# Kernel optimization log

Measured on AMD Instinct MI355X. Metric: run time of the kernel, lower is better.

## Reference

```python
import jax, jax.numpy as jnp
import numpy as np
from jax.scipy.special import digamma, gammaln

NUM_CLASSES = 3
FOCAL_GAMMA = 2.0
LABEL_SMOOTHING = 0.1
EVIDENTIAL_W = 0.1
CONTRASTIVE_W = 0.1
BOUNDARY_W = 0.15
TRIPLET_W = 0.1
QUALITY_W = 0.1
TRIPLET_MARGIN = 1.5


def setup_inputs() -> dict:
    key = jax.random.key(0)
    k1, k2, k3 = jax.random.split(key, 3)
    B, D = 4096, 512
    logits = jax.random.normal(k1, (B, NUM_CLASSES), dtype=jnp.float32)
    targets = jax.random.randint(k2, (B,), 0, 3)
    features = jax.random.normal(k3, (B, D), dtype=jnp.float32)
    alpha = jax.random.uniform(jax.random.fold_in(key, 7), (B, NUM_CLASSES), dtype=jnp.float32)
    focal_alpha = jnp.array([1.0, 2.0, 1.5], dtype=jnp.float32)
    class_weights = jnp.array([1.0, 2.0, 1.5], dtype=jnp.float32)
    return {"logits": logits, "targets": targets, "features": features,
            "alpha": alpha, "epoch": 1, "focal_alpha": focal_alpha,
            "class_weights": class_weights}


def reference(logits, targets, features, alpha, epoch, focal_alpha, class_weights):
    B = logits.shape[0]
    C = NUM_CLASSES

    # ---- focal loss (label-smoothed CE, torch semantics) ----
    logp = jax.nn.log_softmax(logits, axis=1)                      # [B,C]
    nll = -jnp.take_along_axis(logp, targets[:, None], axis=1)[:, 0]
    ce_ls = (1.0 - LABEL_SMOOTHING) * nll + LABEL_SMOOTHING * (-logp.mean(axis=1))
    pt = jnp.exp(-ce_ls)
    focal = (focal_alpha[targets] * (1.0 - pt) ** FOCAL_GAMMA * ce_ls).mean()

    # ---- weighted CE (torch weighted mean: sum(w*nll)/sum(w)) ----
    w = class_weights[targets]
    ce = (w * nll).sum() / w.sum()

    # ---- enhanced boundary loss ----
    probs = jax.nn.softmax(logits, axis=1)
    real = targets == 0
    semi = targets == 1
    syn = targets == 2
    rb = jnp.where(real, probs[:, 1] + 0.6 * probs[:, 2], 0.0).sum()
    sb = jnp.where(syn, probs[:, 1] + 0.4 * probs[:, 0], 0.0).sum()
    mb = jnp.where(semi, 1.0 - probs[:, 1] + 0.3 * (probs[:, 0] + probs[:, 2]), 0.0).sum()
    boundary = (rb + sb + 4.5 * mb) / (B + 1e-8)

    total = 0.4 * focal + 0.3 * ce + BOUNDARY_W * boundary

    # ---- normalized features and pairwise cosine-sim matrix ----
    norms = jnp.linalg.norm(features, axis=1, keepdims=True)
    f = features / jnp.maximum(norms, 1e-12)
    sim = f @ f.T                                                  # [B,B]
    same = targets[:, None] == targets[None, :]
    eye = jnp.eye(B, dtype=bool)

    # ---- enhanced contrastive loss ----
    pos = jnp.where(same, (1.0 - sim) ** 2, 0.0).sum()
    neg = jnp.where(~same, jnp.clip(sim - 0.2, 0.0) ** 2, 0.0).sum()
    semi_pair = semi[:, None] & semi[None, :]
    semi_l = jnp.where(semi_pair, (1.0 - sim) ** 2, 0.0).sum()
    contrastive = (pos + neg + 4.0 * semi_l) / (B * B + 1e-8)

    # ---- enhanced triplet loss (batch-hard, vectorized) ----
    d2 = jnp.clip(2.0 - 2.0 * sim, 0.0)
    dist = jnp.sqrt(jnp.where(eye, 1.0, d2))  # diag masked; safe sqrt
    pos_mask = same & ~eye
    neg_mask = ~same
    hp = jnp.max(jnp.where(pos_mask, dist, -jnp.inf), axis=1)
    hn = jnp.min(jnp.where(neg_mask, dist, jnp.inf), axis=1)
    valid = pos_mask.any(axis=1) & neg_mask.any(axis=1)
    margin = TRIPLET_MARGIN * jnp.where(targets == 1, 2.5, 1.0)
    tl = jax.nn.relu(hp - hn + margin)
    cnt = valid.sum()
    triplet = jnp.where(cnt > 0,
                        jnp.where(valid, tl, 0.0).sum() / jnp.maximum(cnt, 1),
                        0.0)

    # ---- quality-invariant loss (upper-tri same-class pairs) ----
    upper = jnp.triu(jnp.ones((B, B), dtype=bool), k=1)
    qmask = same & upper
    npairs = qmask.sum()
    q = jnp.where(qmask, (1.0 - sim) ** 2, 0.0).sum() / jnp.maximum(npairs, 1)
    frac2 = syn.astype(jnp.float32).mean()
    q = q * jnp.where(syn.sum() > 0, 1.0 + 2.5 * frac2, 1.0)
    quality = jnp.where(npairs > 0, q, 0.0)

    # ---- evidential loss ----
    onehot = jax.nn.one_hot(targets, C, dtype=jnp.float32)
    S = alpha.sum(axis=1, keepdims=True) + 1e-8
    likelihood = (onehot * (digamma(S) - digamma(alpha + 1e-8))).sum(axis=1)
    at = onehot + (1.0 - onehot) * alpha
    ats = at.sum(axis=1) + 1e-8
    kl = (gammaln(ats) - gammaln(at + 1e-8).sum(axis=1)
          + ((at - 1.0) * (digamma(at + 1e-8) - digamma(ats[:, None] + 1e-8))).sum(axis=1))
    annealing = min(1.0, (epoch / 25.0) ** 2)
    evidential = likelihood.mean() + annealing * 0.2 * kl.mean()

    total = (total + CONTRASTIVE_W * contrastive + TRIPLET_W * triplet
             + QUALITY_W * quality + EVIDENTIAL_W * evidential)
    return total
```

## Files before the change

kernel.cpp:

```cpp
#include <hip/hip_runtime.h>
#include <hip/hip_bf16.h>
#include <cstdint>

typedef __attribute__((ext_vector_type(8))) __bf16 bf8;
typedef __attribute__((ext_vector_type(4))) float f32x4;

#if defined(__has_builtin)
#if __has_builtin(__builtin_amdgcn_global_load_lds)
#define USE_GLL 1
#endif
#endif
#ifndef USE_GLL
#define USE_GLL 0
#endif

#if USE_GLL
__device__ __forceinline__ void gll16(const __bf16* g, __bf16* l){
  __builtin_amdgcn_global_load_lds(
      (const __attribute__((address_space(1))) void*)g,
      (__attribute__((address_space(3))) void*)l, 16, 0, 0);
}
#endif

__device__ __forceinline__ unsigned mapf(float x){
  unsigned u = __float_as_uint(x);
  return (u & 0x80000000u) ? ~u : (u | 0x80000000u);
}
__device__ __forceinline__ float unmapf(unsigned u){
  return __uint_as_float((u & 0x80000000u) ? (u & 0x7FFFFFFFu) : ~u);
}

__device__ float digammaf_(float x){
  float r = 0.f;
  while (x < 6.f){ r -= 1.f/x; x += 1.f; }
  float inv = 1.f/x, inv2 = inv*inv;
  r += logf(x) - 0.5f*inv
     - inv2*(0.08333333333f - inv2*(0.008333333333f - inv2*0.003968253968f));
  return r;
}

__global__ __launch_bounds__(256) void k_prep(const float* __restrict__ feat,
    __bf16* __restrict__ fb2,
    const float* __restrict__ logits, const int* __restrict__ targets,
    const float* __restrict__ alpha,  const float* __restrict__ fa,
    const float* __restrict__ cw, int B, int D,
    float* __restrict__ psum, unsigned* rowMinU, unsigned* rowMaxU){
  int bid = blockIdx.x, tid = threadIdx.x;
  int wave = tid >> 6, lane = tid & 63;
  __shared__ float sloc[4][8];

  int row = bid*4 + wave;
  const float* src = feat + (size_t)row*D;
  float ss = 0.f;
  for (int c = lane*4; c < D; c += 64*4){
    float4 v = *(const float4*)(src + c);
    ss += v.x*v.x + v.y*v.y + v.z*v.z + v.w*v.w;
  }
  #pragma unroll
  for (int off=32; off; off>>=1) ss += __shfl_xor(ss, off);
  float inv = 1.f / fmaxf(sqrtf(ss), 1e-12f);

  int p = row >> 6, r = row & 63;
  int rsw = (r >> 1) & 3;
  for (int c = lane*8; c < D; c += 64*8){
    float4 v0 = *(const float4*)(src + c);
    float4 v1 = *(const float4*)(src + c + 4);
    bf8 o;
    o[0]=(__bf16)(v0.x*inv); o[1]=(__bf16)(v0.y*inv);
    o[2]=(__bf16)(v0.z*inv); o[3]=(__bf16)(v0.w*inv);
    o[4]=(__bf16)(v1.x*inv); o[5]=(__bf16)(v1.y*inv);
    o[6]=(__bf16)(v1.z*inv); o[7]=(__bf16)(v1.w*inv);
    int cc = c >> 5;
    int cb = (c >> 3) & 3;
    size_t off = (size_t)(p*16 + cc)*2048 + r*32 + ((cb ^ rsw)*8);
    *(bf8*)(fb2 + off) = o;
  }

  if (tid < 4){ rowMinU[bid*4+tid] = 0xFFFFFFFFu; rowMaxU[bid*4+tid] = 0u; }

  int i = row;
  float l0=logits[3*i], l1=logits[3*i+1], l2=logits[3*i+2];
  int t = targets[i];
  float m = fmaxf(l0, fmaxf(l1,l2));
  float e0=expf(l0-m), e1=expf(l1-m), e2=expf(l2-m);
  float se = e0+e1+e2;
  float lse = m + logf(se);
  float lp0=l0-lse, lp1=l1-lse, lp2=l2-lse;
  float lpt = (t==0)?lp0:((t==1)?lp1:lp2);
  float nll = -lpt;
  float ce_ls = 0.9f*nll + 0.1f*(-(lp0+lp1+lp2)*(1.f/3.f));
  float pt = expf(-ce_ls);
  float om = 1.f - pt;
  float focal_i = fa[t]*om*om*ce_ls;
  float w = cw[t];
  float ce_n = w*nll, ce_d = w;
  float p0=e0/se, p1=e1/se, p2=e2/se;
  float bnd;
  if (t==0)      bnd = p1 + 0.6f*p2;
  else if (t==2) bnd = p1 + 0.4f*p0;
  else           bnd = 4.5f*(1.f - p1 + 0.3f*(p0+p2));
  float a0=alpha[3*i], a1=alpha[3*i+1], a2=alpha[3*i+2];
  float S = a0+a1+a2 + 1e-8f;
  float at_ = (t==0)?a0:((t==1)?a1:a2);
  float lik = digammaf_(S) - digammaf_(at_ + 1e-8f);
  float b0 = (t==0)?1.f:a0, b1 = (t==1)?1.f:a1, b2 = (t==2)?1.f:a2;
  float ats = b0+b1+b2 + 1e-8f;
  float psa = digammaf_(ats + 1e-8f);
  float kl = lgammaf(ats)
     - (lgammaf(b0+1e-8f)+lgammaf(b1+1e-8f)+lgammaf(b2+1e-8f))
     + (b0-1.f)*(digammaf_(b0+1e-8f)-psa)
     + (b1-1.f)*(digammaf_(b1+1e-8f)-psa)
     + (b2-1.f)*(digammaf_(b2+1e-8f)-psa);
  if (lane == 0){
    sloc[wave][0]=focal_i; sloc[wave][1]=ce_n; sloc[wave][2]=ce_d;
    sloc[wave][3]=bnd;     sloc[wave][4]=lik;  sloc[wave][5]=kl;
  }
  __syncthreads();
  if (tid < 6)
    psum[bid*8+tid] = sloc[0][tid]+sloc[1][tid]+sloc[2][tid]+sloc[3][tid];
}

__global__ __launch_bounds__(64) void k_pairs(const __bf16* __restrict__ fb2,
    const int* __restrict__ targets, int B, int D,
    float* __restrict__ pairPart, unsigned* rowMinU, unsigned* rowMaxU){
  __shared__ __bf16 sA[2][2048];
  __shared__ __bf16 sB[2][2048];

  int t = blockIdx.x;
  int bx = (int)((sqrtf(8.f*(float)t + 1.f) - 1.f)*0.5f);
  while ((bx+1)*(bx+2)/2 <= t) bx++;
  while (bx*(bx+1)/2 > t) bx--;
  int by = t - bx*(bx+1)/2;
  bool isDiag = (by == bx);
  int rowBase = by*64, colBase = bx*64;

  int lane = threadIdx.x;
  int quad = lane >> 4, l16 = lane & 15;
  int NCH = D/32;

  const __bf16* srcA = fb2 + (size_t)by*NCH*2048 + lane*8;
  const __bf16* srcB = fb2 + (size_t)bx*NCH*2048 + lane*8;
  const __bf16* sB0  = isDiag ? &sA[0][0] : &sB[0][0];

  int offA[4];
  #pragma unroll
  for (int mi=0; mi<4; mi++){
    int R = mi*16 + l16;
    offA[mi] = R*32 + ((quad ^ ((R>>1)&3))*8);
  }

  f32x4 C[4][4] = {};

#if USE_GLL
  #define STAGE(buf, it) do{ \
    const __bf16* ga_ = srcA + (it)*2048; \
    gll16(ga_ + 0*512, &sA[buf][0*512]); \
    gll16(ga_ + 1*512, &sA[buf][1*512]); \
    gll16(ga_ + 2*512, &sA[buf][2*512]); \
    gll16(ga_ + 3*512, &sA[buf][3*512]); \
    if (!isDiag){ \
      const __bf16* gb_ = srcB + (it)*2048; \
      gll16(gb_ + 0*512, &sB[buf][0*512]); \
      gll16(gb_ + 1*512, &sB[buf][1*512]); \
      gll16(gb_ + 2*512, &sB[buf][2*512]); \
      gll16(gb_ + 3*512, &sB[buf][3*512]); \
    } \
  }while(0)
#else
  #define STAGE(buf, it) do{ \
    const __bf16* ga_ = srcA + (it)*2048; \
    _Pragma("unroll") \
    for (int j=0; j<4; j++) \
      *(bf8*)&sA[buf][j*512 + lane*8] = *(const bf8*)(ga_ + j*512); \
    if (!isDiag){ \
      const __bf16* gb_ = srcB + (it)*2048; \
      _Pragma("unroll") \
      for (int j=0; j<4; j++) \
        *(bf8*)&sB[buf][j*512 + lane*8] = *(const bf8*)(gb_ + j*512); \
    } \
  }while(0)
#endif

  #define COMPUTE(buf) do{ \
    bf8 aF[4], bF[4]; \
    _Pragma("unroll") \
    for (int mi=0; mi<4; mi++) aF[mi] = *(const bf8*)(&sA[0][0] + (buf)*2048 + offA[mi]); \
    _Pragma("unroll") \
    for (int ni=0; ni<4; ni++) bF[ni] = *(const bf8*)(sB0 + (buf)*2048 + offA[ni]); \
    _Pragma("unroll") \
    for (int mi=0; mi<4; mi++) \
      _Pragma("unroll") \
      for (int ni=0; ni<4; ni++) \
        C[mi][ni] = __builtin_amdgcn_mfma_f32_16x16x32_bf16(aF[mi], bF[ni], C[mi][ni], 0,0,0); \
  }while(0)

  STAGE(0, 0);
  for (int it=0; it<NCH; it+=2){
    STAGE(1, it+1);
    COMPUTE(0);
    if (it+2 < NCH) STAGE(0, it+2);
    COMPUTE(1);
  }

  int tcol[4];
  #pragma unroll
  for (int ni=0; ni<4; ni++) tcol[ni] = targets[colBase + ni*16 + l16];

  float pos=0.f, neg=0.f, semi=0.f, diag=0.f;
  float cmin[4], cmax[4];
  #pragma unroll
  for (int ni=0; ni<4; ni++){ cmin[ni]=2.f; cmax[ni]=-2.f; }

  #pragma unroll
  for (int mi=0; mi<4; mi++){
    #pragma unroll
    for (int r=0; r<4; r++){
      int rl = mi*16 + quad*4 + r;
      int row = rowBase + rl;
      int tr = targets[row];
      float vmin = 2.f, vmax = -2.f;
      #pragma unroll
      for (int ni=0; ni<4; ni++){
        int col = colBase + ni*16 + l16;
        float s = C[mi][ni][r];
        if (tr == tcol[ni]){
          float omv = 1.f - s;
          float q = omv*omv;
          pos += q;
          if (tr == 1) semi += q;
          if (row == col) diag += q;
          else {
            vmin = fminf(vmin, s);
            cmin[ni] = fminf(cmin[ni], s);
          }
        } else {
          float c0 = fmaxf(s - 0.2f, 0.f);
          neg += c0*c0;
          vmax = fmaxf(vmax, s);
          cmax[ni] = fmaxf(cmax[ni], s);
        }
      }
      #pragma unroll
      for (int off=1; off<16; off<<=1){
        vmin = fminf(vmin, __shfl_xor(vmin, off));
        vmax = fmaxf(vmax, __shfl_xor(vmax, off));
      }
      if (l16 == 0){
        atomicMin(&rowMinU[row], mapf(vmin));
        atomicMax(&rowMaxU[row], mapf(vmax));
      }
    }
  }

  if (!isDiag){
    #pragma unroll
    for (int ni=0; ni<4; ni++){
      float cn = cmin[ni], cx = cmax[ni];
      cn = fminf(cn, __shfl_xor(cn, 16)); cn = fminf(cn, __shfl_xor(cn, 32));
      cx = fmaxf(cx, __shfl_xor(cx, 16)); cx = fmaxf(cx, __shfl_xor(cx, 32));
      if (quad == 0){
        int col = colBase + ni*16 + l16;
        atomicMin(&rowMinU[col], mapf(cn));
        atomicMax(&rowMaxU[col], mapf(cx));
      }
    }
  }

  #pragma unroll
  for (int off=32; off; off>>=1){
    pos  += __shfl_xor(pos, off);
    neg  += __shfl_xor(neg, off);
    semi += __shfl_xor(semi, off);
    diag += __shfl_xor(diag, off);
  }
  if (lane == 0){
    float fac = isDiag ? 1.f : 2.f;
    pairPart[blockIdx.x*4+0] = pos*fac;
    pairPart[blockIdx.x*4+1] = neg*fac;
    pairPart[blockIdx.x*4+2] = semi*fac;
    pairPart[blockIdx.x*4+3] = diag;
  }
}

__global__ __launch_bounds__(1024) void k_final(const int* __restrict__ targets,
    const int* __restrict__ epoch_p, int B, int nprep, int nblk,
    const float* __restrict__ pairPart, const float* __restrict__ psum,
    const unsigned* rowMinU, const unsigned* rowMaxU, float* out){
  int tid = threadIdx.x, wave = tid>>6, lane = tid&63;
  __shared__ float redf[16][8];
  __shared__ int   redi[16][4];
  __shared__ float tot6[6];
  __shared__ int   cns[3];
  __shared__ float ptot[4];

  {
    int c0=0,c1=0,c2=0;
    for (int i4 = tid; i4 < B/4; i4 += 1024){
      int4 tv = ((const int4*)targets)[i4];
      c0 += (tv.x==0)+(tv.y==0)+(tv.z==0)+(tv.w==0);
      c1 += (tv.x==1)+(tv.y==1)+(tv.z==1)+(tv.w==1);
      c2 += (tv.x==2)+(tv.y==2)+(tv.z==2)+(tv.w==2);
    }
    #pragma unroll
    for (int off=32; off; off>>=1){
      c0+=__shfl_xor(c0,off); c1+=__shfl_xor(c1,off); c2+=__shfl_xor(c2,off);
    }
    if (lane==0){ redi[wave][0]=c0; redi[wave][1]=c1; redi[wave][2]=c2; }
  }
  {
    float v0=0,v1=0,v2=0,v3=0,v4=0,v5=0;
    for (int s = tid; s < nprep; s += 1024){
      float4 a = *(const float4*)(psum + s*8);
      float4 b = *(const float4*)(psum + s*8 + 4);
      v0+=a.x; v1+=a.y; v2+=a.z; v3+=a.w; v4+=b.x; v5+=b.y;
    }
    #pragma unroll
    for (int off=32; off; off>>=1){
      v0+=__shfl_xor(v0,off); v1+=__shfl_xor(v1,off); v2+=__shfl_xor(v2,off);
      v3+=__shfl_xor(v3,off); v4+=__shfl_xor(v4,off); v5+=__shfl_xor(v5,off);
    }
    if (lane==0){
      redf[wave][0]=v0; redf[wave][1]=v1; redf[wave][2]=v2;
      redf[wave][3]=v3; redf[wave][4]=v4; redf[wave][5]=v5;
    }
  }
  __syncthreads();
  if (tid == 0){
    int c0=0,c1=0,c2=0;
    float v[6]={0,0,0,0,0,0};
    for (int w2=0; w2<16; w2++){
      c0+=redi[w2][0]; c1+=redi[w2][1]; c2+=redi[w2][2];
      for (int j=0;j<6;j++) v[j]+=redf[w2][j];
    }
    cns[0]=c0; cns[1]=c1; cns[2]=c2;
    for (int j=0;j<6;j++) tot6[j]=v[j];
  }
  __syncthreads();

  {
    float p=0,n=0,s2=0,d=0;
    for (int s = tid; s < nblk; s += 1024){
      float4 a = *(const float4*)(pairPart + s*4);
      p+=a.x; n+=a.y; s2+=a.z; d+=a.w;
    }
    #pragma unroll
    for (int off=32; off; off>>=1){
      p+=__shfl_xor(p,off); n+=__shfl_xor(n,off);
      s2+=__shfl_xor(s2,off); d+=__shfl_xor(d,off);
    }
    if (lane==0){ redf[wave][0]=p; redf[wave][1]=n; redf[wave][2]=s2; redf[wave][3]=d; }
  }
  __syncthreads();
  if (tid == 0){
    float a=0,b=0,c=0,e=0;
    for (int w2=0; w2<16; w2++){ a+=redf[w2][0]; b+=redf[w2][1]; c+=redf[w2][2]; e+=redf[w2][3]; }
    ptot[0]=a; ptot[1]=b; ptot[2]=c; ptot[3]=e;
  }
  __syncthreads();

  int n0=cns[0], n1=cns[1], n2=cns[2];

  float tsum = 0.f, tcnt = 0.f;
  for (int i = tid; i < B; i += 1024){
    int t = targets[i];
    int nt = (t==0)?n0:((t==1)?n1:n2);
    if (nt - 1 > 0 && B - nt > 0){
      float mn = unmapf(rowMinU[i]);
      float mx = unmapf(rowMaxU[i]);
      float hp = sqrtf(fmaxf(2.f - 2.f*mn, 0.f));
      float hn = sqrtf(fmaxf(2.f - 2.f*mx, 0.f));
      float margin = 1.5f * ((t==1) ? 2.5f : 1.f);
      float tl = fmaxf(hp - hn + margin, 0.f);
      tsum += tl; tcnt += 1.f;
    }
  }
  #pragma unroll
  for (int off=32; off; off>>=1){ tsum += __shfl_xor(tsum, off); tcnt += __shfl_xor(tcnt, off); }
  if (lane==0){ redf[wave][6]=tsum; redf[wave][7]=tcnt; }
  __syncthreads();

  if (tid==0){
    float ts=0, tn=0;
    for (int w2=0; w2<16; w2++){ ts+=redf[w2][6]; tn+=redf[w2][7]; }
    float triplet = (tn > 0.f) ? ts / fmaxf(tn, 1.f) : 0.f;
    float pos=ptot[0], neg=ptot[1], semi=ptot[2], diag=ptot[3];
    float Bf = (float)B;
    float focal = tot6[0] / Bf;
    float ce = tot6[1] / tot6[2];
    float boundary = tot6[3] / (Bf + 1e-8f);
    float contrastive = (pos + neg + 4.f*semi) / (Bf*Bf + 1e-8f);
    long long npl = ((long long)n0*(n0-1) + (long long)n1*(n1-1) + (long long)n2*(n2-1))/2;
    float qsum = (pos - diag) * 0.5f;
    float q = qsum / (float)(npl > 0 ? npl : 1);
    if (n2 > 0) q *= (1.f + 2.5f * ((float)n2 / Bf));
    float quality = (npl > 0) ? q : 0.f;
    int ep = epoch_p[0];
    float er = (float)ep / 25.f;
    float ann = fminf(1.f, er*er);
    float evidential = tot6[4]/Bf + ann*0.2f*tot6[5]/Bf;
    float total = 0.4f*focal + 0.3f*ce + 0.15f*boundary
                + 0.1f*contrastive + 0.1f*triplet + 0.1f*quality + 0.1f*evidential;
    out[0] = total;
  }
}

extern "C" void kernel_launch(void* const* d_in, const int* in_sizes, int n_in,
                              void* d_out, int out_size, void* d_ws, size_t ws_size,
                              hipStream_t stream){
  const float* logits   = (const float*)d_in[0];
  const int*   targets  = (const int*)d_in[1];
  const float* features = (const float*)d_in[2];
  const float* alpha    = (const float*)d_in[3];
  const int*   epoch    = (const int*)d_in[4];
  const float* fa       = (const float*)d_in[5];
  const float* cw       = (const float*)d_in[6];
  int B = in_sizes[1];
  int D = in_sizes[2] / B;
  int nprep = B/4;
  int T  = B / 64;
  int nblk = T*(T+1)/2;

  char* ws = (char*)d_ws;
  float*    psum     = (float*)(ws);
  float*    pairPart = (float*)(ws + 65536);
  unsigned* rowMinU  = (unsigned*)(ws + 131072);
  unsigned* rowMaxU  = (unsigned*)(ws + 131072 + (size_t)B*4);
  __bf16*   fb2      = (__bf16*)(ws + 131072 + (size_t)B*8);

  k_prep <<<nprep, 256, 0, stream>>>(features, fb2, logits, targets, alpha, fa, cw,
                                     B, D, psum, rowMinU, rowMaxU);
  k_pairs<<<nblk, 64, 0, stream>>>(fb2, targets, B, D, pairPart, rowMinU, rowMaxU);
  k_final<<<1, 1024, 0, stream>>>(targets, epoch, B, nprep, nblk, pairPart, psum,
                                  rowMinU, rowMaxU, (float*)d_out);
}
```

Baseline: 120.1 us.

## Pre-permute features into MFMA fragment order and load directly to registers

The prep kernel now writes normalized bf16 features in a layout matching the MFMA operand fragment order, so the pair kernel can load fragments straight from global memory into registers with double-buffered register prefetch and skip LDS staging. This removes the shared-memory round trip and the global_load_lds path, and adds s_setprio around the MFMA blocks. The per-row loss terms in the prep kernel are computed only by 4 lanes of wave 0 and reduced with shuffles instead of an LDS array and __syncthreads. The tradeoff is that operand reuse now relies on the L1/L2 caches rather than LDS, and register pressure grows.

```diff
diff --git a/kernel.cpp b/kernel.cpp
--- a/kernel.cpp
+++ b/kernel.cpp
@@ -4,23 +4,6 @@
 
 typedef __attribute__((ext_vector_type(8))) __bf16 bf8;
 typedef __attribute__((ext_vector_type(4))) float f32x4;
-
-#if defined(__has_builtin)
-#if __has_builtin(__builtin_amdgcn_global_load_lds)
-#define USE_GLL 1
-#endif
-#endif
-#ifndef USE_GLL
-#define USE_GLL 0
-#endif
-
-#if USE_GLL
-__device__ __forceinline__ void gll16(const __bf16* g, __bf16* l){
-  __builtin_amdgcn_global_load_lds(
-      (const __attribute__((address_space(1))) void*)g,
-      (__attribute__((address_space(3))) void*)l, 16, 0, 0);
-}
-#endif
 
 __device__ __forceinline__ unsigned mapf(float x){
   unsigned u = __float_as_uint(x);
@@ -47,7 +30,6 @@
     float* __restrict__ psum, unsigned* rowMinU, unsigned* rowMaxU){
   int bid = blockIdx.x, tid = threadIdx.x;
   int wave = tid >> 6, lane = tid & 63;
-  __shared__ float sloc[4][8];
 
   int row = bid*4 + wave;
   const float* src = feat + (size_t)row*D;
@@ -61,7 +43,8 @@
   float inv = 1.f / fmaxf(sqrtf(ss), 1e-12f);
 
   int p = row >> 6, r = row & 63;
-  int rsw = (r >> 1) & 3;
+  int mi = r >> 4, l16r = r & 15;
+  int NCH = D >> 5;
   for (int c = lane*8; c < D; c += 64*8){
     float4 v0 = *(const float4*)(src + c);
     float4 v1 = *(const float4*)(src + c + 4);
@@ -71,61 +54,67 @@
     o[4]=(__bf16)(v1.x*inv); o[5]=(__bf16)(v1.y*inv);
     o[6]=(__bf16)(v1.z*inv); o[7]=(__bf16)(v1.w*inv);
     int cc = c >> 5;
-    int cb = (c >> 3) & 3;
-    size_t off = (size_t)(p*16 + cc)*2048 + r*32 + ((cb ^ rsw)*8);
+    int q  = (c >> 3) & 3;
+    size_t off = ((((size_t)p*NCH + cc)*4 + mi)*64 + l16r*4 + q)*8;
     *(bf8*)(fb2 + off) = o;
   }
 
   if (tid < 4){ rowMinU[bid*4+tid] = 0xFFFFFFFFu; rowMaxU[bid*4+tid] = 0u; }
 
-  int i = row;
-  float l0=logits[3*i], l1=logits[3*i+1], l2=logits[3*i+2];
-  int t = targets[i];
-  float m = fmaxf(l0, fmaxf(l1,l2));
-  float e0=expf(l0-m), e1=expf(l1-m), e2=expf(l2-m);
-  float se = e0+e1+e2;
-  float lse = m + logf(se);
-  float lp0=l0-lse, lp1=l1-lse, lp2=l2-lse;
-  float lpt = (t==0)?lp0:((t==1)?lp1:lp2);
-  float nll = -lpt;
-  float ce_ls = 0.9f*nll + 0.1f*(-(lp0+lp1+lp2)*(1.f/3.f));
-  float pt = expf(-ce_ls);
-  float om = 1.f - pt;
-  float focal_i = fa[t]*om*om*ce_ls;
-  float w = cw[t];
-  float ce_n = w*nll, ce_d = w;
-  float p0=e0/se, p1=e1/se, p2=e2/se;
-  float bnd;
-  if (t==0)      bnd = p1 + 0.6f*p2;
-  else if (t==2) bnd = p1 + 0.4f*p0;
-  else           bnd = 4.5f*(1.f - p1 + 0.3f*(p0+p2));
-  float a0=alpha[3*i], a1=alpha[3*i+1], a2=alpha[3*i+2];
-  float S = a0+a1+a2 + 1e-8f;
-  float at_ = (t==0)?a0:((t==1)?a1:a2);
-  float lik = digammaf_(S) - digammaf_(at_ + 1e-8f);
-  float b0 = (t==0)?1.f:a0, b1 = (t==1)?1.f:a1, b2 = (t==2)?1.f:a2;
-  float ats = b0+b1+b2 + 1e-8f;
-  float psa = digammaf_(ats + 1e-8f);
-  float kl = lgammaf(ats)
-     - (lgammaf(b0+1e-8f)+lgammaf(b1+1e-8f)+lgammaf(b2+1e-8f))
-     + (b0-1.f)*(digammaf_(b0+1e-8f)-psa)
-     + (b1-1.f)*(digammaf_(b1+1e-8f)-psa)
-     + (b2-1.f)*(digammaf_(b2+1e-8f)-psa);
-  if (lane == 0){
-    sloc[wave][0]=focal_i; sloc[wave][1]=ce_n; sloc[wave][2]=ce_d;
-    sloc[wave][3]=bnd;     sloc[wave][4]=lik;  sloc[wave][5]=kl;
-  }
-  __syncthreads();
-  if (tid < 6)
-    psum[bid*8+tid] = sloc[0][tid]+sloc[1][tid]+sloc[2][tid]+sloc[3][tid];
+  if (wave == 0){
+    float r0=0.f,r1=0.f,r2=0.f,r3=0.f,r4=0.f,r5=0.f;
+    if (lane < 4){
+      int i = bid*4 + lane;
+      float l0=logits[3*i], l1=logits[3*i+1], l2=logits[3*i+2];
+      int t = targets[i];
+      float m = fmaxf(l0, fmaxf(l1,l2));
+      float e0=expf(l0-m), e1=expf(l1-m), e2=expf(l2-m);
+      float se = e0+e1+e2;
+      float lse = m + logf(se);
+      float lp0=l0-lse, lp1=l1-lse, lp2=l2-lse;
+      float lpt = (t==0)?lp0:((t==1)?lp1:lp2);
+      float nll = -lpt;
+      float ce_ls = 0.9f*nll + 0.1f*(-(lp0+lp1+lp2)*(1.f/3.f));
+      float pt = expf(-ce_ls);
+      float om = 1.f - pt;
+      float focal_i = fa[t]*om*om*ce_ls;
+      float w = cw[t];
+      float ce_n = w*nll, ce_d = w;
+      float p0=e0/se, p1=e1/se, p2=e2/se;
+      float bnd;
+      if (t==0)      bnd = p1 + 0.6f*p2;
+      else if (t==2) bnd = p1 + 0.4f*p0;
+      else           bnd = 4.5f*(1.f - p1 + 0.3f*(p0+p2));
+      float a0=alpha[3*i], a1=alpha[3*i+1], a2=alpha[3*i+2];
+      float S = a0+a1+a2 + 1e-8f;
+      float at_ = (t==0)?a0:((t==1)?a1:a2);
+      float lik = digammaf_(S) - digammaf_(at_ + 1e-8f);
+      float b0 = (t==0)?1.f:a0, b1 = (t==1)?1.f:a1, b2 = (t==2)?1.f:a2;
+      float ats = b0+b1+b2 + 1e-8f;
+      float psa = digammaf_(ats + 1e-8f);
+      float kl = lgammaf(ats)
+         - (lgammaf(b0+1e-8f)+lgammaf(b1+1e-8f)+lgammaf(b2+1e-8f))
+         + (b0-1.f)*(digammaf_(b0+1e-8f)-psa)
+         + (b1-1.f)*(digammaf_(b1+1e-8f)-psa)
+         + (b2-1.f)*(digammaf_(b2+1e-8f)-psa);
+      r0=focal_i; r1=ce_n; r2=ce_d; r3=bnd; r4=lik; r5=kl;
+    }
+    float s0 = ((__shfl(r0,0)+__shfl(r0,1))+__shfl(r0,2))+__shfl(r0,3);
+    float s1 = ((__shfl(r1,0)+__shfl(r1,1))+__shfl(r1,2))+__shfl(r1,3);
+    float s2 = ((__shfl(r2,0)+__shfl(r2,1))+__shfl(r2,2))+__shfl(r2,3);
+    float s3 = ((__shfl(r3,0)+__shfl(r3,1))+__shfl(r3,2))+__shfl(r3,3);
+    float s4 = ((__shfl(r4,0)+__shfl(r4,1))+__shfl(r4,2))+__shfl(r4,3);
+    float s5 = ((__shfl(r5,0)+__shfl(r5,1))+__shfl(r5,2))+__shfl(r5,3);
+    if (lane == 0){
+      psum[bid*8+0]=s0; psum[bid*8+1]=s1; psum[bid*8+2]=s2;
+      psum[bid*8+3]=s3; psum[bid*8+4]=s4; psum[bid*8+5]=s5;
+    }
+  }
 }
 
 __global__ __launch_bounds__(64) void k_pairs(const __bf16* __restrict__ fb2,
     const int* __restrict__ targets, int B, int D,
     float* __restrict__ pairPart, unsigned* rowMinU, unsigned* rowMaxU){
-  __shared__ __bf16 sA[2][2048];
-  __shared__ __bf16 sB[2][2048];
-
   int t = blockIdx.x;
   int bx = (int)((sqrtf(8.f*(float)t + 1.f) - 1.f)*0.5f);
   while ((bx+1)*(bx+2)/2 <= t) bx++;
@@ -136,71 +125,41 @@
 
   int lane = threadIdx.x;
   int quad = lane >> 4, l16 = lane & 15;
-  int NCH = D/32;
-
-  const __bf16* srcA = fb2 + (size_t)by*NCH*2048 + lane*8;
-  const __bf16* srcB = fb2 + (size_t)bx*NCH*2048 + lane*8;
-  const __bf16* sB0  = isDiag ? &sA[0][0] : &sB[0][0];
-
-  int offA[4];
-  #pragma unroll
-  for (int mi=0; mi<4; mi++){
-    int R = mi*16 + l16;
-    offA[mi] = R*32 + ((quad ^ ((R>>1)&3))*8);
-  }
+  int NCH = D >> 5;
+
+  int lperm = (l16*4 + quad)*8;
+  const __bf16* pA = fb2 + (size_t)by*NCH*2048 + lperm;
+  const __bf16* pB = fb2 + (size_t)bx*NCH*2048 + lperm;
 
   f32x4 C[4][4] = {};
-
-#if USE_GLL
-  #define STAGE(buf, it) do{ \
-    const __bf16* ga_ = srcA + (it)*2048; \
-    gll16(ga_ + 0*512, &sA[buf][0*512]); \
-    gll16(ga_ + 1*512, &sA[buf][1*512]); \
-    gll16(ga_ + 2*512, &sA[buf][2*512]); \
-    gll16(ga_ + 3*512, &sA[buf][3*512]); \
-    if (!isDiag){ \
-      const __bf16* gb_ = srcB + (it)*2048; \
-      gll16(gb_ + 0*512, &sB[buf][0*512]); \
-      gll16(gb_ + 1*512, &sB[buf][1*512]); \
-      gll16(gb_ + 2*512, &sB[buf][2*512]); \
-      gll16(gb_ + 3*512, &sB[buf][3*512]); \
-    } \
+  bf8 A0[4], B0[4], A1[4], B1[4];
+
+  #define LOADF(AD, BD, it) do{ \
+    _Pragma("unroll") \
+    for (int m=0; m<4; m++) AD[m] = *(const bf8*)(pA + (size_t)((it)*4 + m)*512); \
+    _Pragma("unroll") \
+    for (int m=0; m<4; m++) BD[m] = *(const bf8*)(pB + (size_t)((it)*4 + m)*512); \
   }while(0)
-#else
-  #define STAGE(buf, it) do{ \
-    const __bf16* ga_ = srcA + (it)*2048; \
-    _Pragma("unroll") \
-    for (int j=0; j<4; j++) \
-      *(bf8*)&sA[buf][j*512 + lane*8] = *(const bf8*)(ga_ + j*512); \
-    if (!isDiag){ \
-      const __bf16* gb_ = srcB + (it)*2048; \
-      _Pragma("unroll") \
-      for (int j=0; j<4; j++) \
-        *(bf8*)&sB[buf][j*512 + lane*8] = *(const bf8*)(gb_ + j*512); \
-    } \
-  }while(0)
-#endif
-
-  #define COMPUTE(buf) do{ \
-    bf8 aF[4], bF[4]; \
-    _Pragma("unroll") \
-    for (int mi=0; mi<4; mi++) aF[mi] = *(const bf8*)(&sA[0][0] + (buf)*2048 + offA[mi]); \
-    _Pragma("unroll") \
-    for (int ni=0; ni<4; ni++) bF[ni] = *(const bf8*)(sB0 + (buf)*2048 + offA[ni]); \
+
+  #define COMPUTE(AF, BF) do{ \
+    __builtin_amdgcn_s_setprio(1); \
     _Pragma("unroll") \
     for (int mi=0; mi<4; mi++) \
       _Pragma("unroll") \
       for (int ni=0; ni<4; ni++) \
-        C[mi][ni] = __builtin_amdgcn_mfma_f32_16x16x32_bf16(aF[mi], bF[ni], C[mi][ni], 0,0,0); \
+        C[mi][ni] = __builtin_amdgcn_mfma_f32_16x16x32_bf16(AF[mi], BF[ni], C[mi][ni], 0,0,0); \
+    __builtin_amdgcn_s_setprio(0); \
   }while(0)
 
-  STAGE(0, 0);
+  LOADF(A0, B0, 0);
   for (int it=0; it<NCH; it+=2){
-    STAGE(1, it+1);
-    COMPUTE(0);
-    if (it+2 < NCH) STAGE(0, it+2);
-    COMPUTE(1);
-  }
+    LOADF(A1, B1, it+1);
+    COMPUTE(A0, B0);
+    if (it+2 < NCH) LOADF(A0, B0, it+2);
+    COMPUTE(A1, B1);
+  }
+  #undef LOADF
+  #undef COMPUTE
 
   int tcol[4];
   #pragma unroll
```

After: 126.7 us. 1.06x slower.

## Remap pair tiles per XCD for L2 locality and slim per-row loss prep

Applied to the files above, without the earlier changes.

The pair-tile kernel now remaps blockIdx so that each of the 8 XCDs, which receive blocks round-robin, gets a contiguous range of triangular tile indices. This is meant to improve L2 reuse of the shared feature tiles. In the prep kernel, the per-row scalar loss work (softmax, digamma, lgamma) moves from every lane of all four waves to four lanes of one wave, reduced with shuffles, which removes redundant transcendental work and a __syncthreads. The NCH stride is also generalized from a hard-coded 16, and outputs are indexed by the logical tile id.

```diff
diff --git a/kernel.cpp b/kernel.cpp
--- a/kernel.cpp
+++ b/kernel.cpp
@@ -47,7 +47,6 @@
     float* __restrict__ psum, unsigned* rowMinU, unsigned* rowMaxU){
   int bid = blockIdx.x, tid = threadIdx.x;
   int wave = tid >> 6, lane = tid & 63;
-  __shared__ float sloc[4][8];
 
   int row = bid*4 + wave;
   const float* src = feat + (size_t)row*D;
@@ -62,6 +61,7 @@
 
   int p = row >> 6, r = row & 63;
   int rsw = (r >> 1) & 3;
+  int NCH = D >> 5;
   for (int c = lane*8; c < D; c += 64*8){
     float4 v0 = *(const float4*)(src + c);
     float4 v1 = *(const float4*)(src + c + 4);
@@ -72,61 +72,74 @@
     o[6]=(__bf16)(v1.z*inv); o[7]=(__bf16)(v1.w*inv);
     int cc = c >> 5;
     int cb = (c >> 3) & 3;
-    size_t off = (size_t)(p*16 + cc)*2048 + r*32 + ((cb ^ rsw)*8);
+    size_t off = (size_t)(p*NCH + cc)*2048 + r*32 + ((cb ^ rsw)*8);
     *(bf8*)(fb2 + off) = o;
   }
 
   if (tid < 4){ rowMinU[bid*4+tid] = 0xFFFFFFFFu; rowMaxU[bid*4+tid] = 0u; }
 
-  int i = row;
-  float l0=logits[3*i], l1=logits[3*i+1], l2=logits[3*i+2];
-  int t = targets[i];
-  float m = fmaxf(l0, fmaxf(l1,l2));
-  float e0=expf(l0-m), e1=expf(l1-m), e2=expf(l2-m);
-  float se = e0+e1+e2;
-  float lse = m + logf(se);
-  float lp0=l0-lse, lp1=l1-lse, lp2=l2-lse;
-  float lpt = (t==0)?lp0:((t==1)?lp1:lp2);
-  float nll = -lpt;
-  float ce_ls = 0.9f*nll + 0.1f*(-(lp0+lp1+lp2)*(1.f/3.f));
-  float pt = expf(-ce_ls);
-  float om = 1.f - pt;
-  float focal_i = fa[t]*om*om*ce_ls;
-  float w = cw[t];
-  float ce_n = w*nll, ce_d = w;
-  float p0=e0/se, p1=e1/se, p2=e2/se;
-  float bnd;
-  if (t==0)      bnd = p1 + 0.6f*p2;
-  else if (t==2) bnd = p1 + 0.4f*p0;
-  else           bnd = 4.5f*(1.f - p1 + 0.3f*(p0+p2));
-  float a0=alpha[3*i], a1=alpha[3*i+1], a2=alpha[3*i+2];
-  float S = a0+a1+a2 + 1e-8f;
-  float at_ = (t==0)?a0:((t==1)?a1:a2);
-  float lik = digammaf_(S) - digammaf_(at_ + 1e-8f);
-  float b0 = (t==0)?1.f:a0, b1 = (t==1)?1.f:a1, b2 = (t==2)?1.f:a2;
-  float ats = b0+b1+b2 + 1e-8f;
-  float psa = digammaf_(ats + 1e-8f);
-  float kl = lgammaf(ats)
-     - (lgammaf(b0+1e-8f)+lgammaf(b1+1e-8f)+lgammaf(b2+1e-8f))
-     + (b0-1.f)*(digammaf_(b0+1e-8f)-psa)
-     + (b1-1.f)*(digammaf_(b1+1e-8f)-psa)
-     + (b2-1.f)*(digammaf_(b2+1e-8f)-psa);
-  if (lane == 0){
-    sloc[wave][0]=focal_i; sloc[wave][1]=ce_n; sloc[wave][2]=ce_d;
-    sloc[wave][3]=bnd;     sloc[wave][4]=lik;  sloc[wave][5]=kl;
-  }
-  __syncthreads();
-  if (tid < 6)
-    psum[bid*8+tid] = sloc[0][tid]+sloc[1][tid]+sloc[2][tid]+sloc[3][tid];
+  if (wave == 0){
+    float r0=0.f,r1=0.f,r2=0.f,r3=0.f,r4=0.f,r5=0.f;
+    if (lane < 4){
+      int i = bid*4 + lane;
+      float l0=logits[3*i], l1=logits[3*i+1], l2=logits[3*i+2];
+      int t = targets[i];
+      float m = fmaxf(l0, fmaxf(l1,l2));
+      float e0=expf(l0-m), e1=expf(l1-m), e2=expf(l2-m);
+      float se = e0+e1+e2;
+      float lse = m + logf(se);
+      float lp0=l0-lse, lp1=l1-lse, lp2=l2-lse;
+      float lpt = (t==0)?lp0:((t==1)?lp1:lp2);
+      float nll = -lpt;
+      float ce_ls = 0.9f*nll + 0.1f*(-(lp0+lp1+lp2)*(1.f/3.f));
+      float pt = expf(-ce_ls);
+      float om = 1.f - pt;
+      float focal_i = fa[t]*om*om*ce_ls;
+      float w = cw[t];
+      float ce_n = w*nll, ce_d = w;
+      float p0=e0/se, p1=e1/se, p2=e2/se;
+      float bnd;
+      if (t==0)      bnd = p1 + 0.6f*p2;
+      else if (t==2) bnd = p1 + 0.4f*p0;
+      else           bnd = 4.5f*(1.f - p1 + 0.3f*(p0+p2));
+      float a0=alpha[3*i], a1=alpha[3*i+1], a2=alpha[3*i+2];
+      float S = a0+a1+a2 + 1e-8f;
+      float at_ = (t==0)?a0:((t==1)?a1:a2);
+      float lik = digammaf_(S) - digammaf_(at_ + 1e-8f);
+      float b0 = (t==0)?1.f:a0, b1 = (t==1)?1.f:a1, b2 = (t==2)?1.f:a2;
+      float ats = b0+b1+b2 + 1e-8f;
+      float psa = digammaf_(ats + 1e-8f);
+      float kl = lgammaf(ats)
+         - (lgammaf(b0+1e-8f)+lgammaf(b1+1e-8f)+lgammaf(b2+1e-8f))
+         + (b0-1.f)*(digammaf_(b0+1e-8f)-psa)
+         + (b1-1.f)*(digammaf_(b1+1e-8f)-psa)
+         + (b2-1.f)*(digammaf_(b2+1e-8f)-psa);
+      r0=focal_i; r1=ce_n; r2=ce_d; r3=bnd; r4=lik; r5=kl;
+    }
+    float s0 = ((__shfl(r0,0)+__shfl(r0,1))+__shfl(r0,2))+__shfl(r0,3);
+    float s1 = ((__shfl(r1,0)+__shfl(r1,1))+__shfl(r1,2))+__shfl(r1,3);
+    float s2 = ((__shfl(r2,0)+__shfl(r2,1))+__shfl(r2,2))+__shfl(r2,3);
+    float s3 = ((__shfl(r3,0)+__shfl(r3,1))+__shfl(r3,2))+__shfl(r3,3);
+    float s4 = ((__shfl(r4,0)+__shfl(r4,1))+__shfl(r4,2))+__shfl(r4,3);
+    float s5 = ((__shfl(r5,0)+__shfl(r5,1))+__shfl(r5,2))+__shfl(r5,3);
+    if (lane == 0){
+      psum[bid*8+0]=s0; psum[bid*8+1]=s1; psum[bid*8+2]=s2;
+      psum[bid*8+3]=s3; psum[bid*8+4]=s4; psum[bid*8+5]=s5;
+    }
+  }
 }
 
 __global__ __launch_bounds__(64) void k_pairs(const __bf16* __restrict__ fb2,
-    const int* __restrict__ targets, int B, int D,
+    const int* __restrict__ targets, int B, int D, int nblk,
     float* __restrict__ pairPart, unsigned* rowMinU, unsigned* rowMaxU){
   __shared__ __bf16 sA[2][2048];
   __shared__ __bf16 sB[2][2048];
 
-  int t = blockIdx.x;
+  int raw = blockIdx.x;
+  int q8 = nblk >> 3, r8 = nblk & 7;
+  int xcd = raw & 7, o8 = raw >> 3;
+  int t = (xcd < r8 ? xcd*(q8+1) : r8*(q8+1) + (xcd-r8)*q8) + o8;
+
   int bx = (int)((sqrtf(8.f*(float)t + 1.f) - 1.f)*0.5f);
   while ((bx+1)*(bx+2)/2 <= t) bx++;
   while (bx*(bx+1)/2 > t) bx--;
@@ -201,6 +214,8 @@
     if (it+2 < NCH) STAGE(0, it+2);
     COMPUTE(1);
   }
+  #undef STAGE
+  #undef COMPUTE
 
   int tcol[4];
   #pragma unroll
@@ -275,10 +290,10 @@
   }
   if (lane == 0){
     float fac = isDiag ? 1.f : 2.f;
-    pairPart[blockIdx.x*4+0] = pos*fac;
-    pairPart[blockIdx.x*4+1] = neg*fac;
-    pairPart[blockIdx.x*4+2] = semi*fac;
-    pairPart[blockIdx.x*4+3] = diag;
+    pairPart[t*4+0] = pos*fac;
+    pairPart[t*4+1] = neg*fac;
+    pairPart[t*4+2] = semi*fac;
+    pairPart[t*4+3] = diag;
   }
 }
 
@@ -429,7 +444,8 @@
 
   k_prep <<<nprep, 256, 0, stream>>>(features, fb2, logits, targets, alpha, fa, cw,
                                      B, D, psum, rowMinU, rowMaxU);
-  k_pairs<<<nblk, 64, 0, stream>>>(fb2, targets, B, D, pairPart, rowMinU, rowMaxU);
+  k_pairs<<<nblk, 64, 0, stream>>>(fb2, targets, B, D, nblk, pairPart,
+                                   rowMinU, rowMaxU);
   k_final<<<1, 1024, 0, stream>>>(targets, epoch, B, nprep, nblk, pairPart, psum,
                                   rowMinU, rowMaxU, (float*)d_out);
 }
```

Measured after the change: 123.3 us. +2.7%, slower.
